# Performance work log

Measured on AMD Instinct MI355X. Metric: run time of the kernel, lower is better.

Reference implementation:

```python
import jax, jax.numpy as jnp
from jax import lax
import numpy as np

Z, Y, X = 41, 256, 256  # sparse_shape = grid_size[::-1]
N_VOX = 60000
C_IN = 4
DN = ('NCDHW', 'OIDHW', 'NCDHW')


def _conv(x, w, stride=(1, 1, 1), pad=1):
    return lax.conv_general_dilated(x, w, stride, [(pad, pad)] * 3, dimension_numbers=DN)


def _tconv(x, w, stride=(2, 2, 2), pad=1, outpad=(0, 0, 0)):
    # torch ConvTranspose3d (weight [Cin,Cout,k,k,k]) == conv with lhs dilation,
    # spatially-flipped, in/out-swapped kernel, padding (k-1-p, k-1-p+output_padding)
    wt = jnp.flip(jnp.swapaxes(w, 0, 1), axis=(2, 3, 4))
    padding = [(2 - pad, 2 - pad + op) for op in outpad]  # k=3
    return lax.conv_general_dilated(x, wt, (1, 1, 1), padding, lhs_dilation=stride, dimension_numbers=DN)


def _bn_relu(y, s, b, m):
    # eval-mode BN folded into per-channel scale/shift, then ReLU, then restrict
    # to the sparse active-site mask (spconv only stores features at active sites)
    return jax.nn.relu(y * s[None, :, None, None, None] + b[None, :, None, None, None]) * m


def _forward(feats, params, coords, batch_size):
    (w1, s1, b1, w2a, s2a, b2a, w2b, s2b, b2b, w3a, s3a, b3a, w3b, s3b, b3b,
     w4a, s4a, b4a, w4b, s4b, b4b, w5a, s5a, b5a, w5b, s5b, b5b) = params
    B = batch_size
    bi, zi, yi, xi = coords[:, 0], coords[:, 1], coords[:, 2], coords[:, 3]
    dense = jnp.zeros((B, C_IN, Z, Y, X), feats.dtype).at[bi, :, zi, yi, xi].set(feats)
    m0 = jnp.zeros((B, 1, Z, Y, X), feats.dtype).at[bi, 0, zi, yi, xi].set(1.0)
    one = jnp.ones((1, 1, 3, 3, 3), feats.dtype)
    # conv1: SparseConv3d k3 s1 p1 -> active set dilates
    m1 = (_conv(m0, one) > 0).astype(feats.dtype)
    x = _bn_relu(_conv(dense, w1), s1, b1, m1)
    # conv2: SparseConv3d s2 + SubMConv3d (mask unchanged for subm)
    m2 = (_conv(m1, one, (2, 2, 2)) > 0).astype(feats.dtype)
    x = _bn_relu(_conv(x, w2a, (2, 2, 2)), s2a, b2a, m2)
    x = _bn_relu(_conv(x, w2b), s2b, b2b, m2)
    # conv3
    m3 = (_conv(m2, one, (2, 2, 2)) > 0).astype(feats.dtype)
    x = _bn_relu(_conv(x, w3a, (2, 2, 2)), s3a, b3a, m3)
    x = _bn_relu(_conv(x, w3b), s3b, b3b, m3)
    # deconv4: SparseConvTranspose3d s2 + subm
    m4 = (_tconv(m3, one) > 0).astype(feats.dtype)
    x = _bn_relu(_tconv(x, w4a), s4a, b4a, m4)
    x = _bn_relu(_conv(x, w4b), s4b, b4b, m4)
    # deconv5: output_padding (0,3,3) restores full Y/X resolution
    m5 = (_tconv(m4, one, outpad=(0, 3, 3)) > 0).astype(feats.dtype)
    x = _bn_relu(_tconv(x, w5a, outpad=(0, 3, 3)), s5a, b5a, m5)
    x = _bn_relu(_conv(x, w5b), s5b, b5b, m5)
    return x  # dense [B, 32, Z, Y, X]; zeros at inactive sites


def setup_inputs() -> dict:
    rng = np.random.default_rng(0)
    flat = rng.choice(Z * Y * X, size=N_VOX, replace=False)
    zi = (flat // (Y * X)).astype(np.int32)
    rem = flat % (Y * X)
    yi = (rem // X).astype(np.int32)
    xi = (rem % X).astype(np.int32)
    coords = np.stack([np.zeros(N_VOX, np.int32), zi, yi, xi], axis=1)

    def w(o, i):
        return jnp.asarray((rng.standard_normal((o, i, 3, 3, 3)) * 0.05).astype(np.float32))

    def scale(c):
        return jnp.asarray(rng.uniform(0.5, 1.5, c).astype(np.float32))

    def shift(c):
        return jnp.asarray((rng.standard_normal(c) * 0.1).astype(np.float32))

    return {
        'occ_voxel_features': jnp.asarray(rng.standard_normal((N_VOX, C_IN)).astype(np.float32)),
        'occ_voxel_coords': jnp.asarray(coords),
        'batch_size': 1,
        'w1': w(16, 4), 's1': scale(16), 'b1': shift(16),
        'w2a': w(32, 16), 's2a': scale(32), 'b2a': shift(32),
        'w2b': w(32, 32), 's2b': scale(32), 'b2b': shift(32),
        'w3a': w(64, 32), 's3a': scale(64), 'b3a': shift(64),
        'w3b': w(64, 64), 's3b': scale(64), 'b3b': shift(64),
        'w4a': w(64, 32), 's4a': scale(32), 'b4a': shift(32),  # transpose weight [Cin,Cout,...]
        'w4b': w(32, 32), 's4b': scale(32), 'b4b': shift(32),
        'w5a': w(32, 32), 's5a': scale(32), 'b5a': shift(32),
        'w5b': w(32, 32), 's5b': scale(32), 'b5b': shift(32),
    }


def reference(occ_voxel_features, occ_voxel_coords, batch_size,
              w1, s1, b1, w2a, s2a, b2a, w2b, s2b, b2b,
              w3a, s3a, b3a, w3b, s3b, b3b,
              w4a, s4a, b4a, w4b, s4b, b4b,
              w5a, s5a, b5a, w5b, s5b, b5b):
    params = (w1, s1, b1, w2a, s2a, b2a, w2b, s2b, b2b, w3a, s3a, b3a, w3b, s3b, b3b,
              w4a, s4a, b4a, w4b, s4b, b4b, w5a, s5a, b5a, w5b, s5b, b5b)
    return _forward(occ_voxel_features, params, occ_voxel_coords, batch_size)
```

## Files before the change

### kernel.cpp

```cpp
#include <hip/hip_runtime.h>
#include <hip/hip_bf16.h>
#include <stdint.h>

namespace {

constexpr int Z0 = 41, Y0 = 256, X0 = 256;
constexpr int Z2 = 21, Y2 = 128, X2 = 128;
constexpr int Z3 = 11, Y3 = 64,  X3 = 64;
constexpr int Z4 = 21, Y4 = 127, X4 = 127;
constexpr int NV0 = Z0 * Y0 * X0;
constexpr int NV2 = Z2 * Y2 * X2;
constexpr int NV3 = Z3 * Y3 * X3;
constexpr int NV4 = Z4 * Y4 * X4;

constexpr int ZP0 = 43, YP0 = 258, XP0 = 258; constexpr int NP0 = ZP0 * YP0 * XP0;
constexpr int ZP2 = 23, YP2 = 130, XP2 = 130; constexpr int NP2 = ZP2 * YP2 * XP2;
constexpr int ZP3 = 13, YP3 = 66,  XP3 = 66;  constexpr int NP3 = ZP3 * YP3 * XP3;
constexpr int ZP4 = 23, YP4 = 129, XP4 = 129; constexpr int NP4 = ZP4 * YP4 * XP4;

using bf16 = __hip_bfloat16;
typedef __attribute__((ext_vector_type(8))) short s16x8;
typedef __attribute__((ext_vector_type(4))) float f32x4;
typedef __attribute__((ext_vector_type(16))) float f32x16;
typedef __attribute__((ext_vector_type(4))) unsigned u32x4;

__device__ inline unsigned f2b(float f) {
    return (unsigned)__builtin_bit_cast(unsigned short, __float2bfloat16(f));
}

__device__ inline int xcd_swz(int bid, int nwg) {
    int q = nwg >> 3, r = nwg & 7;
    int x = bid & 7, j = bid >> 3;
    return (x < r ? x * (q + 1) : r * (q + 1) + (x - r) * q) + j;
}

__device__ inline void glds16(const bf16* g, void* l) {
    __builtin_amdgcn_global_load_lds(
        (const __attribute__((address_space(1))) void*)g,
        (__attribute__((address_space(3))) void*)l, 16, 0, 0);
}

__global__ __launch_bounds__(256) void sentinel_k(float* out) { out[0] = 12345.0f; }

__global__ __launch_bounds__(256) void scatter_k(const float* __restrict__ feats,
                                                 const int* __restrict__ coords,
                                                 bf16* __restrict__ dense,
                                                 uint8_t* __restrict__ m0, int n) {
    int v = blockIdx.x * 256 + threadIdx.x;
    if (v >= n) return;
    int z = coords[v * 4 + 1], y = coords[v * 4 + 2], x = coords[v * 4 + 3];
    m0[(z * Y0 + y) * X0 + x] = 1;
    int pp = ((z + 1) * YP0 + (y + 1)) * XP0 + (x + 1);
    uint2 u;
    u.x = f2b(feats[v * 4 + 0]) | (f2b(feats[v * 4 + 1]) << 16);
    u.y = f2b(feats[v * 4 + 2]) | (f2b(feats[v * 4 + 3]) << 16);
    *(uint2*)(dense + (size_t)pp * 4) = u;
}

template <int C>
__global__ __launch_bounds__(256) void halo_zero_k(bf16* __restrict__ buf,
                                                   int Zi, int Yi, int Xi,
                                                   int Zp, int Yp, int Xp) {
    int i = blockIdx.x * 256 + threadIdx.x;
    int tot = Zp * Yp * Xp;
    if (i >= tot) return;
    int x = i % Xp; int t = i / Xp; int y = t % Yp; int z = t / Yp;
    bool halo = (z < 1) | (z > Zi) | (y < 1) | (y > Yi) | (x < 1) | (x > Xi);
    if (!halo) return;
    uint4 zz = make_uint4(0, 0, 0, 0);
    uint4* p = (uint4*)(buf + (size_t)i * C);
#pragma unroll
    for (int j = 0; j < C / 8; ++j) p[j] = zz;
}

__global__ __launch_bounds__(256) void repack_frag_k(const float* __restrict__ w,
                                                     bf16* __restrict__ wf,
                                                     int CIN, int COUT, int TRANS) {
    int NT = COUT / 16, KT = CIN / 32;
    int i = blockIdx.x * 256 + threadIdx.x;
    int total = 27 * NT * KT * 64;
    if (i >= total) return;
    int lane = i & 63; int t = i >> 6;
    int kt = t % KT; t /= KT; int nt = t % NT; int tap = t / NT;
    int co = nt * 16 + (lane & 15);
    int ci0 = kt * 32 + (lane >> 4) * 8;
    unsigned e[8];
#pragma unroll
    for (int j = 0; j < 8; ++j) {
        int ci = ci0 + j;
        int src = TRANS ? ((ci * COUT + co) * 27 + tap) : ((co * CIN + ci) * 27 + tap);
        e[j] = f2b(w[src]);
    }
    uint4 u;
    u.x = e[0] | (e[1] << 16); u.y = e[2] | (e[3] << 16);
    u.z = e[4] | (e[5] << 16); u.w = e[6] | (e[7] << 16);
    ((uint4*)wf)[i] = u;
}

__global__ __launch_bounds__(256) void repack_frag32_k(const float* __restrict__ w,
                                                       bf16* __restrict__ wf) {
    int i = blockIdx.x * 256 + threadIdx.x;
    if (i >= 27 * 2 * 64) return;
    int lane = i & 63; int t2 = i >> 6;
    int ks = t2 & 1; int tap = t2 >> 1;
    int co = lane & 31; int h = lane >> 5;
    unsigned e[8];
#pragma unroll
    for (int j = 0; j < 8; ++j) {
        int cin = ks * 16 + h * 8 + j;
        e[j] = f2b(w[(co * 32 + cin) * 27 + tap]);
    }
    uint4 u;
    u.x = e[0] | (e[1] << 16); u.y = e[2] | (e[3] << 16);
    u.z = e[4] | (e[5] << 16); u.w = e[6] | (e[7] << 16);
    ((uint4*)wf)[i] = u;
}

__global__ __launch_bounds__(256) void repack_frag_c16_k(const float* __restrict__ w,
                                                         bf16* __restrict__ wf) {
    int i = blockIdx.x * 256 + threadIdx.x;
    int total = 14 * 2 * 64;
    if (i >= total) return;
    int lane = i & 63; int t = i >> 6;
    int nt = t & 1; int p = t >> 1;
    int lg = lane >> 4, lr = lane & 15;
    int co = nt * 16 + lr;
    unsigned e[8];
#pragma unroll
    for (int j = 0; j < 8; ++j) {
        int tap = 2 * p + (lg >> 1);
        int ci = (lg & 1) * 8 + j;
        e[j] = (tap < 27) ? f2b(w[(co * 16 + ci) * 27 + tap]) : 0u;
    }
    uint4 u;
    u.x = e[0] | (e[1] << 16); u.y = e[2] | (e[3] << 16);
    u.z = e[4] | (e[5] << 16); u.w = e[6] | (e[7] << 16);
    ((uint4*)wf)[i] = u;
}

__global__ __launch_bounds__(256) void repack_frag_l1_k(const float* __restrict__ w,
                                                        bf16* __restrict__ wf) {
    int i = blockIdx.x * 256 + threadIdx.x;
    if (i >= 256) return;
    int lane = i & 63, kb = i >> 6;
    int lg = lane >> 4, lr = lane & 15;
    unsigned e[8];
#pragma unroll
    for (int j = 0; j < 8; ++j) {
        int tap = kb * 8 + lg * 2 + (j >> 2);
        int ci = j & 3;
        e[j] = (tap < 27) ? f2b(w[(lr * 4 + ci) * 27 + tap]) : 0u;
    }
    uint4 u;
    u.x = e[0] | (e[1] << 16); u.y = e[2] | (e[3] << 16);
    u.z = e[4] | (e[5] << 16); u.w = e[6] | (e[7] << 16);
    ((uint4*)wf)[i] = u;
}

__global__ __launch_bounds__(256) void dilate_k(const uint8_t* __restrict__ in,
                                                uint8_t* __restrict__ out,
                                                int Zi, int Yi, int Xi,
                                                int Zo, int Yo, int Xo, int stride) {
    int idx = blockIdx.x * 256 + threadIdx.x;
    int total = Zo * Yo * Xo;
    if (idx >= total) return;
    int x = idx % Xo; int t = idx / Xo; int y = t % Yo; int z = t / Yo;
    int YX = Yi * Xi;
    uint8_t r = 0;
    for (int kz = 0; kz < 3; ++kz) {
        int zi = z * stride + kz - 1;
        if ((unsigned)zi >= (unsigned)Zi) continue;
        for (int ky = 0; ky < 3; ++ky) {
            int yi = y * stride + ky - 1;
            if ((unsigned)yi >= (unsigned)Yi) continue;
            for (int kx = 0; kx < 3; ++kx) {
                int xi = x * stride + kx - 1;
                if ((unsigned)xi >= (unsigned)Xi) continue;
                r |= in[zi * YX + yi * Xi + xi];
            }
        }
    }
    out[idx] = r ? 1 : 0;
}

__global__ __launch_bounds__(256) void dilate4_k(const uint8_t* __restrict__ in,
                                                 uint8_t* __restrict__ out,
                                                 int Z, int Y, int X) {
    int ngx = X >> 2;
    int g = blockIdx.x * 256 + threadIdx.x;
    int total = Z * Y * ngx;
    if (g >= total) return;
    int gx = g % ngx; int t = g / ngx; int y = t % Y; int z = t / Y;
    const int YX = Y * X;
    unsigned r = 0;
    for (int kz = 0; kz < 3; ++kz) {
        int zi = z + kz - 1;
        if ((unsigned)zi >= (unsigned)Z) continue;
        for (int ky = 0; ky < 3; ++ky) {
            int yi = y + ky - 1;
            if ((unsigned)yi >= (unsigned)Y) continue;
            const unsigned* rw = (const unsigned*)(in + zi * YX + yi * X);
            unsigned u1 = rw[gx];
            unsigned u0 = gx ? rw[gx - 1] : 0u;
            unsigned u2 = (gx + 1 < ngx) ? rw[gx + 1] : 0u;
            r |= u1 | ((u1 << 8) | (u0 >> 24)) | ((u1 >> 8) | (u2 << 24));
        }
    }
    r |= r >> 4; r |= r >> 2; r |= r >> 1; r &= 0x01010101u;
    ((unsigned*)out)[g] = r;
}

__global__ __launch_bounds__(256) void tdilate_k(const uint8_t* __restrict__ in,
                                                 uint8_t* __restrict__ out,
                                                 int Zi, int Yi, int Xi,
                                                 int Zo, int Yo, int Xo) {
    int idx = blockIdx.x * 256 + threadIdx.x;
    int total = Zo * Yo * Xo;
    if (idx >= total) return;
    int x = idx % Xo; int t = idx / Xo; int y = t % Yo; int z = t / Yo;
    int YX = Yi * Xi;
    uint8_t r = 0;
    for (int kz = 0; kz < 3; ++kz) {
        int tz = z + 1 - kz;
        if (tz & 1) continue;
        int zi = tz >> 1;
        if ((unsigned)zi >= (unsigned)Zi) continue;
        for (int ky = 0; ky < 3; ++ky) {
            int ty = y + 1 - ky;
            if (ty & 1) continue;
            int yi = ty >> 1;
            if ((unsigned)yi >= (unsigned)Yi) continue;
            for (int kx = 0; kx < 3; ++kx) {
                int tx = x + 1 - kx;
                if (tx & 1) continue;
                int xi = tx >> 1;
                if ((unsigned)xi >= (unsigned)Xi) continue;
                r |= in[zi * YX + yi * Xi + xi];
            }
        }
    }
    out[idx] = r ? 1 : 0;
}

__global__ __launch_bounds__(256) void tdilate4_k(const uint8_t* __restrict__ in,
                                                  uint8_t* __restrict__ out,
                                                  int Zi, int Yi, int Xi,
                                                  int Zo, int Yo, int Xo) {
    int ngx = Xo >> 2;
    int g = blockIdx.x * 256 + threadIdx.x;
    int total = Zo * Yo * ngx;
    if (g >= total) return;
    int gx = g % ngx; int t = g / ngx; int y = t % Yo; int z = t / Yo;
    int YX = Yi * Xi;
    int j0 = gx * 2;
    unsigned r0 = 0, r1 = 0, r2 = 0, r3 = 0;
    for (int kz = 0; kz < 3; ++kz) {
        int tz = z + 1 - kz;
        if (tz & 1) continue;
        int zi = tz >> 1;
        if ((unsigned)zi >= (unsigned)Zi) continue;
        for (int ky = 0; ky < 3; ++ky) {
            int ty = y + 1 - ky;
            if (ty & 1) continue;
            int yi = ty >> 1;
            if ((unsigned)yi >= (unsigned)Yi) continue;
            const uint8_t* rp = in + zi * YX + yi * Xi;
            unsigned b0 = (j0 < Xi) ? rp[j0] : 0u;
            unsigned b1 = (j0 + 1 < Xi) ? rp[j0 + 1] : 0u;
            unsigned b2 = (j0 + 2 < Xi) ? rp[j0 + 2] : 0u;
            r0 |= b0; r1 |= b0 | b1; r2 |= b1; r3 |= b1 | b2;
        }
    }
    unsigned rr = (r0 ? 1u : 0u) | (r1 ? 0x100u : 0u) | (r2 ? 0x10000u : 0u) | (r3 ? 0x1000000u : 0u);
    ((unsigned*)out)[g] = rr;
}

__global__ __launch_bounds__(256, 1) void conv_roll_k(
    const bf16* __restrict__ in, const bf16* __restrict__ wfrag,
    const float* __restrict__ scale, const float* __restrict__ shift,
    const uint8_t* __restrict__ mask, float* __restrict__ outf) {
    constexpr int ROWB = 2176;
    constexpr int SLABB = 24576;
    __shared__ uint4 ring4[4 * SLABB / 16];
    char* ring = (char*)ring4;

    const int bid = xcd_swz(blockIdx.x, gridDim.x);
    const int tx = bid & 7;
    const int t2 = bid >> 3;
    const int ty = t2 & 31;
    const int zs = t2 >> 5;
    const int y0 = ty * 8, x0 = tx * 32;
    const int zlo = zs ? 21 : 0;
    const int zcnt = zs ? 20 : 21;

    const int tid = threadIdx.x;
    const int w = tid >> 6, lane = tid & 63;
    const int vx = lane & 31, h = lane >> 5;

#pragma unroll
    for (int k = 0; k < 14; ++k) {
        int base = k * 256 + w * 64;
        if (base < 27 * 2 * 64)
            glds16(wfrag + (size_t)(base + lane) * 8, ring + base * 16);
    }
    asm volatile("s_waitcnt vmcnt(0)" ::: "memory");
    __syncthreads();

    u32x4 breg[27][2];
#pragma unroll
    for (int t = 0; t < 27; ++t) {
        breg[t][0] = *(const u32x4*)(ring + (t * 2 + 0) * 1024 + lane * 16);
        breg[t][1] = *(const u32x4*)(ring + (t * 2 + 1) * 1024 + lane * 16);
    }
    __syncthreads();

    int soff[6];
#pragma unroll
    for (int k = 0; k < 6; ++k) {
        int i = tid + k * 256;
        int ii = i < 1360 ? i : 0;
        int row = ii / 136, c = ii - row * 136;
        int ks = c / 68, r2 = c - ks * 68, hh = r2 / 34, v = r2 - hh * 34;
        soff[k] = ((y0 + row) * XP0 + (x0 + v)) * 32 + (2 * ks + hh) * 8;
    }
    auto stagefn = [&](int p, char* slab) {
        int zp = p < ZP0 ? p : ZP0 - 1;
        const bf16* pb = in + (size_t)zp * ((size_t)YP0 * XP0 * 32);
#pragma unroll
        for (int k = 0; k < 6; ++k)
            glds16(pb + soff[k], slab + (k * 256 + w * 64) * 16);
    };

    int rb[4];
#pragma unroll
    for (int fr = 0; fr < 4; ++fr)
        rb[fr] = (2 * w + fr) * ROWB + h * 544 + vx * 16;

    const float sc = scale[vx], sh = shift[vx];

    stagefn(zlo + 0, ring);
    stagefn(zlo + 1, ring + SLABB);
    stagefn(zlo + 2, ring + 2 * SLABB);
    asm volatile("s_waitcnt vmcnt(0)" ::: "memory");
    __builtin_amdgcn_s_barrier();

    int s0 = 0;
    for (int zi = 0; zi < zcnt; ++zi) {
        const int z = zlo + zi;
        stagefn(z + 3, ring + ((s0 + 3) & 3) * SLABB);

        unsigned mk0[4], mk1[4];
        {
            const uint8_t* mr0 = mask + ((size_t)z * Y0 + (y0 + 2 * w)) * X0 + x0 + 4 * h;
            const uint8_t* mr1 = mr0 + X0;
            mk0[0] = *(const unsigned*)(mr0);      mk0[1] = *(const unsigned*)(mr0 + 8);
            mk0[2] = *(const unsigned*)(mr0 + 16); mk0[3] = *(const unsigned*)(mr0 + 24);
            mk1[0] = *(const unsigned*)(mr1);      mk1[1] = *(const unsigned*)(mr1 + 8);
            mk1[2] = *(const unsigned*)(mr1 + 16); mk1[3] = *(const unsigned*)(mr1 + 24);
        }

        const char* slp0 = ring + s0 * SLABB;
        const char* slp1 = ring + ((s0 + 1) & 3) * SLABB;
        const char* slp2 = ring + ((s0 + 2) & 3) * SLABB;

        f32x16 acc0, acc1;
#pragma unroll
        for (int i = 0; i < 16; ++i) { acc0[i] = 0.f; acc1[i] = 0.f; }

#pragma unroll
        for (int dz = 0; dz < 3; ++dz) {
            const char* slab = dz == 0 ? slp0 : (dz == 1 ? slp1 : slp2);
#pragma unroll
            for (int dx = 0; dx < 3; ++dx) {
#pragma unroll
                for (int ks = 0; ks < 2; ++ks) {
                    const int ko = ks * 1088 + dx * 16;
                    u32x4 a0 = *(const u32x4*)(slab + rb[0] + ko);
                    u32x4 a1 = *(const u32x4*)(slab + rb[1] + ko);
                    u32x4 a2 = *(const u32x4*)(slab + rb[2] + ko);
                    u32x4 a3 = *(const u32x4*)(slab + rb[3] + ko);
                    const int t0 = dz * 9 + 0 * 3 + dx;
                    const int t1 = dz * 9 + 1 * 3 + dx;
                    const int t2_ = dz * 9 + 2 * 3 + dx;
                    acc0 = __builtin_amdgcn_mfma_f32_32x32x16_bf16(
                        __builtin_bit_cast(s16x8, a0), __builtin_bit_cast(s16x8, breg[t0][ks]), acc0, 0, 0, 0);
                    acc1 = __builtin_amdgcn_mfma_f32_32x32x16_bf16(
                        __builtin_bit_cast(s16x8, a1), __builtin_bit_cast(s16x8, breg[t0][ks]), acc1, 0, 0, 0);
                    acc0 = __builtin_amdgcn_mfma_f32_32x32x16_bf16(
                        __builtin_bit_cast(s16x8, a1), __builtin_bit_cast(s16x8, breg[t1][ks]), acc0, 0, 0, 0);
                    acc1 = __builtin_amdgcn_mfma_f32_32x32x16_bf16(
                        __builtin_bit_cast(s16x8, a2), __builtin_bit_cast(s16x8, breg[t1][ks]), acc1, 0, 0, 0);
                    acc0 = __builtin_amdgcn_mfma_f32_32x32x16_bf16(
                        __builtin_bit_cast(s16x8, a2), __builtin_bit_cast(s16x8, breg[t2_][ks]), acc0, 0, 0, 0);
                    acc1 = __builtin_amdgcn_mfma_f32_32x32x16_bf16(
                        __builtin_bit_cast(s16x8, a3), __builtin_bit_cast(s16x8, breg[t2_][ks]), acc1, 0, 0, 0);
                }
            }
        }

        const size_t ob0 = (size_t)vx * NV0 + ((size_t)z * Y0 + (y0 + 2 * w)) * X0 + x0 + 4 * h;
        const size_t ob1 = ob0 + X0;
#pragma unroll
        for (int q = 0; q < 4; ++q) {
            f32x4 o0, o1;
#pragma unroll
            for (int r = 0; r < 4; ++r) {
                float m0 = (float)((mk0[q] >> (8 * r)) & 1);
                float m1 = (float)((mk1[q] >> (8 * r)) & 1);
                o0[r] = fmaxf(fmaf(acc0[q * 4 + r], sc, sh), 0.f) * m0;
                o1[r] = fmaxf(fmaf(acc1[q * 4 + r], sc, sh), 0.f) * m1;
            }
            *(f32x4*)(outf + ob0 + 8 * q) = o0;
            *(f32x4*)(outf + ob1 + 8 * q) = o1;
        }

        asm volatile("s_waitcnt vmcnt(8)" ::: "memory");
        __builtin_amdgcn_s_barrier();
        s0 = (s0 + 1) & 3;
    }
}

__global__ __launch_bounds__(256, 3) void tconv_roll_k(
    const bf16* __restrict__ in, const bf16* __restrict__ wfrag,
    const float* __restrict__ scale, const float* __restrict__ shift,
    const uint8_t* __restrict__ mask, bf16* __restrict__ out,
    int Zo, int Yo, int Xo, int Zi, int Ypi, int Xpi, int Ypo, int Xpo, int nx) {
    constexpr int ROWB = 34 * 64;
    constexpr int SLABB = 3 * ROWB;
    __shared__ uint4 ring4[4 * SLABB / 16];
    char* ring = (char*)ring4;

    const int oct = blockIdx.y;
    const int pz = oct >> 2, py = (oct >> 1) & 1, px = oct & 1;
    const int Zq = (Zo - pz + 1) >> 1;

    const int bid = xcd_swz(blockIdx.x, gridDim.x);
    const int tx = bid % nx, ty = bid / nx;
    const int yq0 = ty * 2, xq0 = tx * 32;

    const int tid = threadIdx.x;
    const int w = tid >> 6, lane = tid & 63;
    const int lg = lane >> 4, lr = lane & 15;
    const int yr = w >> 1, xh = w & 1;

    const int kz0 = pz ? 0 : 1, dzo0 = pz ? 1 : 0;
    const int ky0 = py ? 0 : 1, dyo0 = py ? 1 : 0;
    const int kx0 = px ? 0 : 1, dxo0 = px ? 1 : 0;

    auto stagefn = [&](int p, int slot) {
        if (w < 3) {
            int zs = p < Zi ? p : Zi - 1;
            char* slab = ring + slot * SLABB + w * ROWB;
            const bf16* pb = in + ((size_t)(zs + 1) * Ypi + (yq0 + 1 + w)) * (size_t)Xpi * 32
                                + (size_t)(xq0 + 1) * 32;
            int u0 = lane;      glds16(pb + (u0 ^ ((u0 >> 3) & 7)) * 8, slab);
            int u1 = 64 + lane; glds16(pb + (u1 ^ ((u1 >> 3) & 7)) * 8, slab + 1024);
            if (lane < 8) { int u2 = 128 + lane; glds16(pb + u2 * 8, slab + 2048); }
        }
    };

    const uint4* gw = (const uint4*)wfrag;
    uint4 breg[2][2][2][2];
#pragma unroll
    for (int iz = 0; iz < 2; ++iz) {
        int kz = iz ? 2 : kz0;
#pragma unroll
        for (int iy = 0; iy < 2; ++iy) {
            int ky = iy ? 2 : ky0;
#pragma unroll
            for (int ix = 0; ix < 2; ++ix) {
                int kx = ix ? 2 : kx0;
                int tap = kz * 9 + ky * 3 + kx;
                breg[iz][iy][ix][0] = gw[(tap * 2 + 0) * 64 + lane];
                breg[iz][iy][ix][1] = gw[(tap * 2 + 1) * 64 + lane];
            }
        }
    }

    int b0 = (xh * 16 + lr + dxo0) * 64 + lg * 16;
    int b1 = (xh * 16 + lr) * 64 + lg * 16;
    const int aswA = b0 ^ (((b0 >> 7) & 7) << 4);
    const int aswB = b1 ^ (((b1 >> 7) & 7) << 4);
    const int rowA = (yr + dyo0) * ROWB;
    const int rowB = yr * ROWB;

    const float sc0 = scale[lr], sh0 = shift[lr];
    const float sc1 = scale[16 + lr], sh1 = shift[16 + lr];

    const int yout = 2 * (yq0 + yr) + py;
    const int xb = 2 * (xq0 + xh * 16 + lg * 4) + px;

    stagefn(0, 0); stagefn(1, 1); stagefn(2, 2);
    uint2 mv;
    mv = *(const uint2*)(mask + ((size_t)pz * Yo + yout) * Xo + (xb - px));
    asm volatile("s_waitcnt vmcnt(0)" ::: "memory");
    __builtin_amdgcn_s_barrier();

    int rs0 = 0, wslot = 3;
    for (int zq = 0; zq < Zq; ++zq) {
        uint2 nv;
        {
            int zqn = (zq + 1 < Zq) ? zq + 1 : Zq - 1;
            nv = *(const uint2*)(mask + ((size_t)(2 * zqn + pz) * Yo + yout) * Xo + (xb - px));
        }
        stagefn(zq + 3, wslot);

        int rs1 = rs0 + 1 < 4 ? rs0 + 1 : 0;
        const char* sl_0 = ring + rs0 * SLABB;
        const char* sl_1 = ring + rs1 * SLABB;
        const char* slz0 = pz ? sl_1 : sl_0;
        const char* slz1 = sl_0;

        f32x4 acc0 = (f32x4){0, 0, 0, 0}, acc1 = (f32x4){0, 0, 0, 0};
#pragma unroll
        for (int iz = 0; iz < 2; ++iz) {
            if (iz > pz) continue;
            const char* slab = iz ? slz1 : slz0;
#pragma unroll
            for (int iy = 0; iy < 2; ++iy) {
                if (iy > py) continue;
                const char* rowp = slab + (iy ? rowB : rowA);
#pragma unroll
                for (int ix = 0; ix < 2; ++ix) {
                    if (ix > px) continue;
                    uint4 a = *(const uint4*)(rowp + (ix ? aswB : aswA));
                    acc0 = __builtin_amdgcn_mfma_f32_16x16x32_bf16(
                        __builtin_bit_cast(s16x8, a),
                        __builtin_bit_cast(s16x8, breg[iz][iy][ix][0]), acc0, 0, 0, 0);
                    acc1 = __builtin_amdgcn_mfma_f32_16x16x32_bf16(
                        __builtin_bit_cast(s16x8, a),
                        __builtin_bit_cast(s16x8, breg[iz][iy][ix][1]), acc1, 0, 0, 0);
                }
            }
        }

        const int zout = 2 * zq + pz;
        const size_t opdbase = ((size_t)(zout + 1) * Ypo + (yout + 1)) * Xpo;
#pragma unroll
        for (int r = 0; r < 4; ++r) {
            unsigned word = (r < 2) ? mv.x : mv.y;
            float m = (float)((word >> (px * 8 + (r & 1) * 16)) & 1);
            float v0 = fmaxf(fmaf(acc0[r], sc0, sh0), 0.f) * m;
            float v1 = fmaxf(fmaf(acc1[r], sc1, sh1), 0.f) * m;
            size_t opd = opdbase + (size_t)(xb + 2 * r + 1);
            out[opd * 32 + lr]      = __float2bfloat16(v0);
            out[opd * 32 + 16 + lr] = __float2bfloat16(v1);
        }

        asm volatile("s_waitcnt vmcnt(20)" ::: "memory");
        __builtin_amdgcn_s_barrier();
        rs0 = rs1;
        wslot = wslot + 1 < 4 ? wslot + 1 : 0;
        mv = nv;
    }
}

template <bool FINAL>
__global__ __launch_bounds__(512, 4) void conv_lds_k(
    const bf16* __restrict__ in, const bf16* __restrict__ wfrag,
    const float* __restrict__ scale, const float* __restrict__ shift,
    const uint8_t* __restrict__ mask, bf16* __restrict__ out, float* __restrict__ outf,
    int Zo, int Yo, int Xo, int Ypi, int Xpi, int Ypo, int Xpo, int nx, int ny) {
    constexpr int ROWB = 34 * 64;
    __shared__ uint4 tile4[36 * ROWB / 16];
    char* tile = (char*)tile4;

    const int No = Zo * Yo * Xo;
    const int bid = xcd_swz(blockIdx.x, gridDim.x);
    int tx = bid % nx; int tt = bid / nx; int ty = tt % ny; int tz = tt / ny;
    const int z0 = tz * 4, y0 = ty * 4, x0 = tx * 32;

    const int tid = threadIdx.x;
    const int w = tid >> 6, lane = tid & 63, lg = lane >> 4, lr = lane & 15;

    int anywork;
    {
        int row = tid >> 5, xl = tid & 31;
        int zz = z0 + (row >> 2), yy = y0 + (row & 3), xx = x0 + xl;
        int ok = (zz < Zo) && (yy < Yo) && (xx < Xo) && mask[((size_t)zz * Yo + yy) * Xo + xx];
        anywork = __syncthreads_or(ok);
    }

    f32x4 acc[4][2];
#pragma unroll
    for (int s = 0; s < 4; ++s) { acc[s][0] = (f32x4){0,0,0,0}; acc[s][1] = (f32x4){0,0,0,0}; }

    if (anywork) {
        const int lsw = (lane ^ ((lane >> 3) & 7)) * 8;
        for (int rr = w; rr < 36; rr += 8) {
            int dz = rr / 6, dy = rr % 6;
            const bf16* g = in + ((size_t)(z0 + dz) * Ypi + (y0 + dy)) * Xpi * 32 + (size_t)x0 * 32;
            char* l = tile + rr * ROWB;
            glds16(g + lsw, l);
            glds16(g + 512 + lsw, l + 1024);
            if (lane < 8) glds16(g + 1024 + lane * 8, l + 2048);
        }
        asm volatile("s_waitcnt vmcnt(0)" ::: "memory");
        __syncthreads();

        int rbB[4], bsw[4][3];
#pragma unroll
        for (int s = 0; s < 4; ++s) {
            int lrow = 2 * w + (s >> 1);
            rbB[s] = ((lrow >> 2) * 6 + (lrow & 3)) * ROWB;
            int xpart = (s & 1) * 16 + lr;
#pragma unroll
            for (int dx = 0; dx < 3; ++dx) {
                int b = (xpart + dx) * 64 + lg * 16;
                bsw[s][dx] = b ^ (((b >> 7) & 7) << 4);
            }
        }

        const uint4* gw = (const uint4*)wfrag;
#pragma unroll 1
        for (int dz = 0; dz < 3; ++dz) {
#pragma unroll
            for (int dy = 0; dy < 3; ++dy) {
                const int rowoff = (dz * 6 + dy) * ROWB;
#pragma unroll
                for (int dx = 0; dx < 3; ++dx) {
                    const int tap = dz * 9 + dy * 3 + dx;
                    uint4 b0 = gw[(tap * 2 + 0) * 64 + lane];
                    uint4 b1 = gw[(tap * 2 + 1) * 64 + lane];
                    uint4 ua[4];
#pragma unroll
                    for (int s = 0; s < 4; ++s)
                        ua[s] = *(const uint4*)(tile + rbB[s] + rowoff + bsw[s][dx]);
#pragma unroll
                    for (int s = 0; s < 4; ++s) {
                        acc[s][0] = __builtin_amdgcn_mfma_f32_16x16x32_bf16(
                            __builtin_bit_cast(s16x8, ua[s]),
                            __builtin_bit_cast(s16x8, b0), acc[s][0], 0, 0, 0);
                        acc[s][1] = __builtin_amdgcn_mfma_f32_16x16x32_bf16(
                            __builtin_bit_cast(s16x8, ua[s]),
                            __builtin_bit_cast(s16x8, b1), acc[s][1], 0, 0, 0);
                    }
                }
            }
        }
    }

#pragma unroll
    for (int s = 0; s < 4; ++s) {
        int lrow = 2 * w + (s >> 1);
        int zz = z0 + (lrow >> 2), yy = y0 + (lrow & 3);
        int xv = x0 + (s & 1) * 16 + lg * 4;
        bool rowok = (zz < Zo) && (yy < Yo);
        if (!rowok) continue;
        size_t idx0 = ((size_t)zz * Yo + yy) * Xo + xv;
        float mm[4];
#pragma unroll
        for (int r = 0; r < 4; ++r)
            mm[r] = (xv + r < Xo && mask[idx0 + r]) ? 1.f : 0.f;
        if constexpr (FINAL) {
#pragma unroll
            for (int nt = 0; nt < 2; ++nt) {
                int co = nt * 16 + lr;
                float sc = scale[co], sh = shift[co];
                f32x4 o;
#pragma unroll
                for (int r = 0; r < 4; ++r)
                    o[r] = fmaxf(fmaf(acc[s][nt][r], sc, sh), 0.f) * mm[r];
                if (xv + 3 < Xo) {
                    *(f32x4*)(outf + (size_t)co * No + idx0) = o;
                } else {
#pragma unroll
                    for (int r = 0; r < 4; ++r)
                        if (xv + r < Xo) outf[(size_t)co * No + idx0 + r] = o[r];
                }
            }
        } else {
            int opd = ((zz + 1) * Ypo + (yy + 1)) * Xpo + (xv + 1);
#pragma unroll
            for (int nt = 0; nt < 2; ++nt) {
                int co = nt * 16 + lr;
                float sc = scale[co], sh = shift[co];
#pragma unroll
                for (int r = 0; r < 4; ++r) {
                    if (xv + r >= Xo) continue;
                    float yv = fmaxf(fmaf(acc[s][nt][r], sc, sh), 0.f) * mm[r];
                    out[(size_t)(opd + r) * 32 + co] = __float2bfloat16(yv);
                }
            }
        }
    }
}

template <int CIN, int COUT, int STRIDE, int BLK, bool FINAL>
__global__ __launch_bounds__(BLK, ((CIN <= 32 && COUT <= 32) ? 4 : 2)) void conv_mfma_k(
    const bf16* __restrict__ in, const bf16* __restrict__ wfrag,
    const float* __restrict__ scale, const float* __restrict__ shift,
    const uint8_t* __restrict__ mask, bf16* __restrict__ out, float* __restrict__ outf,
    int Zo, int Yo, int Xo, int Ypi, int Xpi, int Ypo, int Xpo) {
    constexpr int NT = COUT / 16;
    constexpr int KT = CIN / 32;
    const int No = Zo * Yo * Xo;
    const int bid = xcd_swz(blockIdx.x, gridDim.x);
    const int tid = threadIdx.x;
    const int wv = tid >> 6, lane = tid & 63;
    const int lg = lane >> 4, lr = lane & 15;
    const int v0 = bid * BLK + wv * 64;
    if (v0 >= No) return;

    int vm = v0 + lane;
    bool mw = (vm < No) && (mask[vm] != 0);
    const bool anywork = (__ballot(mw) != 0ull);

    f32x4 acc[4][NT];
#pragma unroll
    for (int s = 0; s < 4; ++s)
#pragma unroll
        for (int nt = 0; nt < NT; ++nt) acc[s][nt] = (f32x4){0.f, 0.f, 0.f, 0.f};

    const uint4* gw = (const uint4*)wfrag;

    if (anywork) {
        int pA[4];
#pragma unroll
        for (int s = 0; s < 4; ++s) {
            int vr = v0 + s * 16 + lr;
            if (vr >= No) vr = 0;
            int zz = vr / (Yo * Xo); int rr = vr - zz * (Yo * Xo);
            int yy = rr / Xo; int xx = rr - yy * Xo;
            pA[s] = (((zz * STRIDE + 1) * Ypi + (yy * STRIDE + 1)) * Xpi + (xx * STRIDE + 1)) * CIN + lg * 8;
        }
#pragma unroll
        for (int tap = 0; tap < 27; ++tap) {
            const int kz = tap / 9, r9 = tap - kz * 9, ky = r9 / 3, kx = r9 - ky * 3;
            const int toff = (((kz - 1) * Ypi + (ky - 1)) * Xpi + (kx - 1)) * CIN;
            uint4 ub[NT][KT];
#pragma unroll
            for (int nt = 0; nt < NT; ++nt)
#pragma unroll
                for (int kt = 0; kt < KT; ++kt)
                    ub[nt][kt] = gw[((tap * NT + nt) * KT + kt) * 64 + lane];
            uint4 ua[4][KT];
#pragma unroll
            for (int s = 0; s < 4; ++s)
#pragma unroll
                for (int kt = 0; kt < KT; ++kt)
                    ua[s][kt] = *(const uint4*)(in + pA[s] + toff + kt * 32);
#pragma unroll
            for (int s = 0; s < 4; ++s)
#pragma unroll
                for (int kt = 0; kt < KT; ++kt)
#pragma unroll
                    for (int nt = 0; nt < NT; ++nt)
                        acc[s][nt] = __builtin_amdgcn_mfma_f32_16x16x32_bf16(
                            __builtin_bit_cast(s16x8, ua[s][kt]),
                            __builtin_bit_cast(s16x8, ub[nt][kt]), acc[s][nt], 0, 0, 0);
        }
    }

#pragma unroll
    for (int s = 0; s < 4; ++s) {
        const int vb = v0 + s * 16 + lg * 4;
        int opd[4]; float mm[4]; bool ok[4];
#pragma unroll
        for (int r = 0; r < 4; ++r) {
            int v = vb + r;
            ok[r] = v < No;
            int vc = ok[r] ? v : 0;
            mm[r] = (ok[r] && mask[vc]) ? 1.f : 0.f;
            int zz = vc / (Yo * Xo); int rr = vc - zz * (Yo * Xo);
            int yy = rr / Xo; int xx = rr - yy * Xo;
            opd[r] = FINAL ? vc : ((zz + 1) * Ypo + (yy + 1)) * Xpo + (xx + 1);
        }
#pragma unroll
        for (int nt = 0; nt < NT; ++nt) {
            int co = nt * 16 + lr;
            float sc = scale[co], sh = shift[co];
#pragma unroll
            for (int r = 0; r < 4; ++r) {
                if (!ok[r]) continue;
                float yv = fmaxf(fmaf(acc[s][nt][r], sc, sh), 0.f) * mm[r];
                if constexpr (FINAL) outf[(size_t)co * No + opd[r]] = yv;
                else out[(size_t)opd[r] * COUT + co] = __float2bfloat16(yv);
            }
        }
    }
}

__global__ __launch_bounds__(256, 4) void conv_s2c16_k(
    const bf16* __restrict__ in, const bf16* __restrict__ wfrag,
    const float* __restrict__ scale, const float* __restrict__ shift,
    const uint8_t* __restrict__ mask, bf16* __restrict__ out,
    int Zo, int Yo, int Xo, int Ypi, int Xpi, int Ypo, int Xpo) {
    const int No = Zo * Yo * Xo;
    const int bid = xcd_swz(blockIdx.x, gridDim.x);
    const int tid = threadIdx.x;
    const int wv = tid >> 6, lane = tid & 63;
    const int lg = lane >> 4, lr = lane & 15;
    const int v0 = bid * 256 + wv * 64;
    if (v0 >= No) return;

    int vm = v0 + lane;
    bool mw = (vm < No) && (mask[vm] != 0);
    const bool anywork = (__ballot(mw) != 0ull);

    f32x4 acc[4][2];
#pragma unroll
    for (int s = 0; s < 4; ++s) { acc[s][0] = (f32x4){0,0,0,0}; acc[s][1] = (f32x4){0,0,0,0}; }

    if (anywork) {
        const uint4* gw = (const uint4*)wfrag;
        const int choff = (lg & 1) * 8;
        const int tb = lg >> 1;
        int toffl[14];
#pragma unroll
        for (int p = 0; p < 14; ++p) {
            int tp = 2 * p + tb;
            if (tp >= 27) tp = 0;
            int kz = tp / 9, r9 = tp - kz * 9, ky = r9 / 3, kx = r9 - ky * 3;
            toffl[p] = ((kz * Ypi + ky) * Xpi + kx) * 16;
        }
        int pA[4];
#pragma unroll
        for (int s = 0; s < 4; ++s) {
            int vr = v0 + s * 16 + lr;
            if (vr >= No) vr = 0;
            int zz = vr / (Yo * Xo); int rr = vr - zz * (Yo * Xo);
            int yy = rr / Xo; int xx = rr - yy * Xo;
            pA[s] = (((zz * 2) * Ypi + (yy * 2)) * Xpi + (xx * 2)) * 16 + choff;
        }
#pragma unroll
        for (int p = 0; p < 14; ++p) {
            uint4 b0 = gw[(p * 2 + 0) * 64 + lane];
            uint4 b1 = gw[(p * 2 + 1) * 64 + lane];
            uint4 ua[4];
#pragma unroll
            for (int s = 0; s < 4; ++s)
                ua[s] = *(const uint4*)(in + pA[s] + toffl[p]);
#pragma unroll
            for (int s = 0; s < 4; ++s) {
                acc[s][0] = __builtin_amdgcn_mfma_f32_16x16x32_bf16(
                    __builtin_bit_cast(s16x8, ua[s]),
                    __builtin_bit_cast(s16x8, b0), acc[s][0], 0, 0, 0);
                acc[s][1] = __builtin_amdgcn_mfma_f32_16x16x32_bf16(
                    __builtin_bit_cast(s16x8, ua[s]),
                    __builtin_bit_cast(s16x8, b1), acc[s][1], 0, 0, 0);
            }
        }
    }

#pragma unroll
    for (int s = 0; s < 4; ++s) {
        const int vb = v0 + s * 16 + lg * 4;
        int opd[4]; float mm[4]; bool ok[4];
#pragma unroll
        for (int r = 0; r < 4; ++r) {
            int v = vb + r;
            ok[r] = v < No;
            int vc = ok[r] ? v : 0;
            mm[r] = (ok[r] && mask[vc]) ? 1.f : 0.f;
            int zz = vc / (Yo * Xo); int rr = vc - zz * (Yo * Xo);
            int yy = rr / Xo; int xx = rr - yy * Xo;
            opd[r] = ((zz + 1) * Ypo + (yy + 1)) * Xpo + (xx + 1);
        }
#pragma unroll
        for (int nt = 0; nt < 2; ++nt) {
            int co = nt * 16 + lr;
            float sc = scale[co], sh = shift[co];
#pragma unroll
            for (int r = 0; r < 4; ++r) {
                if (!ok[r]) continue;
                float yv = fmaxf(fmaf(acc[s][nt][r], sc, sh), 0.f) * mm[r];
                out[(size_t)opd[r] * 32 + co] = __float2bfloat16(yv);
            }
        }
    }
}

template <int CIN, int COUT>
__global__ __launch_bounds__(256, 4) void tconv_mfma_k(
    const bf16* __restrict__ in, const bf16* __restrict__ wfrag,
    const float* __restrict__ scale, const float* __restrict__ shift,
    const uint8_t* __restrict__ mask, bf16* __restrict__ out,
    int Zo, int Yo, int Xo, int Ypi, int Xpi, int Ypo, int Xpo) {
    constexpr int NT = COUT / 16;
    constexpr int KT = CIN / 32;
    const int oct = blockIdx.y;
    const int pz = oct >> 2, py = (oct >> 1) & 1, px = oct & 1;
    const int Zq = (Zo - pz + 1) >> 1, Yq = (Yo - py + 1) >> 1, Xq = (Xo - px + 1) >> 1;
    const int Nq = Zq * Yq * Xq;
    const int YXq = Yq * Xq;
    const int bid = xcd_swz(blockIdx.x, gridDim.x);
    const int tid = threadIdx.x;
    const int wv = tid >> 6, lane = tid & 63;
    const int lg = lane >> 4, lr = lane & 15;
    const int v0 = bid * 256 + wv * 64;
    if (v0 >= Nq) return;

    bool mw = false;
    {
        int q = v0 + lane;
        if (q < Nq) {
            int zq = q / YXq; int rr = q - zq * YXq; int yq = rr / Xq; int xq = rr - yq * Xq;
            int zz = 2 * zq + pz, yy = 2 * yq + py, xx = 2 * xq + px;
            mw = mask[(zz * Yo + yy) * Xo + xx] != 0;
        }
    }
    const bool anywork = (__ballot(mw) != 0ull);

    f32x4 acc[4][NT];
#pragma unroll
    for (int s = 0; s < 4; ++s)
#pragma unroll
        for (int nt = 0; nt < NT; ++nt) acc[s][nt] = (f32x4){0.f, 0.f, 0.f, 0.f};

    const uint4* gw = (const uint4*)wfrag;

    if (anywork) {
        int pA[4];
#pragma unroll
        for (int s = 0; s < 4; ++s) {
            int q = v0 + s * 16 + lr;
            if (q >= Nq) q = 0;
            int zq = q / YXq; int rr = q - zq * YXq; int yq = rr / Xq; int xq = rr - yq * Xq;
            pA[s] = (((zq + 1) * Ypi + (yq + 1)) * Xpi + (xq + 1)) * CIN + lg * 8;
        }
        const int nkz = 1 + pz, nky = 1 + py, nkx = 1 + px;
        for (int iz = 0; iz < nkz; ++iz) {
            const int kz = pz ? (iz ? 2 : 0) : 1;
            const int dz = (pz && !iz) ? 1 : 0;
            for (int iy = 0; iy < nky; ++iy) {
                const int ky = py ? (iy ? 2 : 0) : 1;
                const int dy = (py && !iy) ? 1 : 0;
                for (int ix = 0; ix < nkx; ++ix) {
                    const int kx = px ? (ix ? 2 : 0) : 1;
                    const int dx = (px && !ix) ? 1 : 0;
                    const int tap = kz * 9 + ky * 3 + kx;
                    const int toff = ((dz * Ypi + dy) * Xpi + dx) * CIN;
                    uint4 ub[NT][KT];
#pragma unroll
                    for (int nt = 0; nt < NT; ++nt)
#pragma unroll
                        for (int kt = 0; kt < KT; ++kt)
                            ub[nt][kt] = gw[((tap * NT + nt) * KT + kt) * 64 + lane];
                    uint4 ua[4][KT];
#pragma unroll
                    for (int s = 0; s < 4; ++s)
#pragma unroll
                        for (int kt = 0; kt < KT; ++kt)
                            ua[s][kt] = *(const uint4*)(in + pA[s] + toff + kt * 32);
#pragma unroll
                    for (int s = 0; s < 4; ++s)
#pragma unroll
                        for (int kt = 0; kt < KT; ++kt)
#pragma unroll
                            for (int nt = 0; nt < NT; ++nt)
                                acc[s][nt] = __builtin_amdgcn_mfma_f32_16x16x32_bf16(
                                    __builtin_bit_cast(s16x8, ua[s][kt]),
                                    __builtin_bit_cast(s16x8, ub[nt][kt]), acc[s][nt], 0, 0, 0);
                }
            }
        }
    }

#pragma unroll
    for (int s = 0; s < 4; ++s) {
        const int vb = v0 + s * 16 + lg * 4;
        int opd[4]; float mm[4]; bool ok[4];
#pragma unroll
        for (int r = 0; r < 4; ++r) {
            int q = vb + r;
            ok[r] = q < Nq;
            int qc = ok[r] ? q : 0;
            int zq = qc / YXq; int rr = qc - zq * YXq; int yq = rr / Xq; int xq = rr - yq * Xq;
            int zz = 2 * zq + pz, yy = 2 * yq + py, xx = 2 * xq + px;
            mm[r] = (ok[r] && mask[(zz * Yo + yy) * Xo + xx]) ? 1.f : 0.f;
            opd[r] = ((zz + 1) * Ypo + (yy + 1)) * Xpo + (xx + 1);
        }
#pragma unroll
        for (int nt = 0; nt < NT; ++nt) {
            int co = nt * 16 + lr;
            float sc = scale[co], sh = shift[co];
#pragma unroll
            for (int r = 0; r < 4; ++r) {
                if (!ok[r]) continue;
                float yv = fmaxf(fmaf(acc[s][nt][r], sc, sh), 0.f) * mm[r];
                out[(size_t)opd[r] * COUT + co] = __float2bfloat16(yv);
            }
        }
    }
}

__global__ __launch_bounds__(256, 4) void conv_l1_mfma_k(
    const bf16* __restrict__ in, const bf16* __restrict__ wfrag,
    const float* __restrict__ scale, const float* __restrict__ shift,
    const uint8_t* __restrict__ mask, bf16* __restrict__ out,
    int Zo, int Yo, int Xo, int Ypi, int Xpi, int Ypo, int Xpo) {
    const int No = Zo * Yo * Xo;
    const int bid = xcd_swz(blockIdx.x, gridDim.x);
    const int tid = threadIdx.x;
    const int wv = tid >> 6, lane = tid & 63;
    const int lg = lane >> 4, lr = lane & 15;
    const int v0 = bid * 256 + wv * 64;
    if (v0 >= No) return;

    int vm = v0 + lane;
    bool mw = (vm < No) && (mask[vm] != 0);
    const bool anywork = (__ballot(mw) != 0ull);

    f32x4 acc[4];
#pragma unroll
    for (int s = 0; s < 4; ++s) acc[s] = (f32x4){0.f, 0.f, 0.f, 0.f};

    if (anywork) {
        const uint4* gw = (const uint4*)wfrag;
        uint4 bu[4];
#pragma unroll
        for (int kb = 0; kb < 4; ++kb) bu[kb] = gw[kb * 64 + lane];

        int vtf[4][2];
#pragma unroll
        for (int kb = 0; kb < 4; ++kb)
#pragma unroll
            for (int u = 0; u < 2; ++u) {
                int tp = kb * 8 + lg * 2 + u;
                int kz = tp / 9, r9 = tp - kz * 9, ky = r9 / 3, kx = r9 - ky * 3;
                vtf[kb][u] = (tp < 27) ? (((kz - 1) * Ypi + (ky - 1)) * Xpi + (kx - 1)) : 0;
            }

        int pV[4];
#pragma unroll
        for (int s = 0; s < 4; ++s) {
            int vr = v0 + s * 16 + lr;
            if (vr >= No) vr = 0;
            int zz = vr / (Yo * Xo); int rr = vr - zz * (Yo * Xo);
            int yy = rr / Xo; int xx = rr - yy * Xo;
            pV[s] = ((zz + 1) * Ypi + (yy + 1)) * Xpi + (xx + 1);
        }

#pragma unroll
        for (int kb = 0; kb < 4; ++kb) {
#pragma unroll
            for (int s = 0; s < 4; ++s) {
                uint2 a0 = *(const uint2*)(in + (size_t)(pV[s] + vtf[kb][0]) * 4);
                uint2 a1 = *(const uint2*)(in + (size_t)(pV[s] + vtf[kb][1]) * 4);
                int4 ai; ai.x = a0.x; ai.y = a0.y; ai.z = a1.x; ai.w = a1.y;
                acc[s] = __builtin_amdgcn_mfma_f32_16x16x32_bf16(
                    __builtin_bit_cast(s16x8, ai),
                    __builtin_bit_cast(s16x8, bu[kb]), acc[s], 0, 0, 0);
            }
        }
    }

#pragma unroll
    for (int s = 0; s < 4; ++s) {
        const int vb = v0 + s * 16 + lg * 4;
        int co = lr;
        float sc = scale[co], sh = shift[co];
#pragma unroll
        for (int r = 0; r < 4; ++r) {
            int v = vb + r;
            if (v >= No) continue;
            float mm = mask[v] ? 1.f : 0.f;
            int zz = v / (Yo * Xo); int rr = v - zz * (Yo * Xo);
            int yy = rr / Xo; int xx = rr - yy * Xo;
            int opd = ((zz + 1) * Ypo + (yy + 1)) * Xpo + (xx + 1);
            float yv = fmaxf(fmaf(acc[s][r], sc, sh), 0.f) * mm;
            out[(size_t)opd * 16 + co] = __float2bfloat16(yv);
        }
    }
}

inline int nblk(int n) { return (n + 255) / 256; }
inline int cdiv(int a, int b) { return (a + b - 1) / b; }

}

extern "C" void kernel_launch(void* const* d_in, const int* in_sizes, int n_in,
                              void* d_out, int out_size, void* d_ws, size_t ws_size,
                              hipStream_t stream) {
    const float* feats = (const float*)d_in[0];
    const int* coords = (const int*)d_in[1];
    const int NVOX = in_sizes[0] / 4;

    const float *w1 = (const float*)d_in[3], *s1 = (const float*)d_in[4], *b1 = (const float*)d_in[5];
    const float *w2a = (const float*)d_in[6], *s2a = (const float*)d_in[7], *b2a = (const float*)d_in[8];
    const float *w2b = (const float*)d_in[9], *s2b = (const float*)d_in[10], *b2b = (const float*)d_in[11];
    const float *w3a = (const float*)d_in[12], *s3a = (const float*)d_in[13], *b3a = (const float*)d_in[14];
    const float *w3b = (const float*)d_in[15], *s3b = (const float*)d_in[16], *b3b = (const float*)d_in[17];
    const float *w4a = (const float*)d_in[18], *s4a = (const float*)d_in[19], *b4a = (const float*)d_in[20];
    const float *w4b = (const float*)d_in[21], *s4b = (const float*)d_in[22], *b4b = (const float*)d_in[23];
    const float *w5a = (const float*)d_in[24], *s5a = (const float*)d_in[25], *b5a = (const float*)d_in[26];
    const float *w5b = (const float*)d_in[27], *s5b = (const float*)d_in[28], *b5b = (const float*)d_in[29];

    char* ws = (char*)d_ws;
    size_t off = 0;
    auto alloc = [&](size_t bytes) -> void* {
        void* p = ws + off;
        off = (off + bytes + 255) & ~(size_t)255;
        return p;
    };

    uint8_t* m0 = (uint8_t*)alloc(NV0);
    uint8_t* m1 = (uint8_t*)alloc(NV0);
    uint8_t* m2 = (uint8_t*)alloc(NV2);
    uint8_t* m3 = (uint8_t*)alloc(NV3);
    uint8_t* m4 = (uint8_t*)alloc(NV4);
    uint8_t* m5 = (uint8_t*)alloc(NV0);

    bf16* slot0 = (bf16*)alloc((size_t)NP0 * 32 * 2);
    bf16* slot1 = (bf16*)alloc((size_t)NP0 * 16 * 2);

    bf16* dense0 = slot0;
    bf16* x1     = slot1;
    bf16* x2a    = slot0;
    bf16* x2b    = slot1;
    bf16* x3a    = slot0;
    bf16* x3b    = slot1;
    bf16* x4a    = slot0;
    bf16* x4b    = slot1;
    bf16* x5a    = slot0;

    bf16* wfL1 = (bf16*)alloc(4 * 64 * 8 * 2);
    bf16* wf2a = (bf16*)alloc((size_t)14 * 2 * 64 * 16);
    bf16* wf2b = (bf16*)alloc((size_t)27 * 2 * 1 * 64 * 16);
    bf16* wf3a = (bf16*)alloc((size_t)27 * 4 * 1 * 64 * 16);
    bf16* wf3b = (bf16*)alloc((size_t)27 * 4 * 2 * 64 * 16);
    bf16* wf4a = (bf16*)alloc((size_t)27 * 2 * 2 * 64 * 16);
    bf16* wf4b = (bf16*)alloc((size_t)27 * 2 * 1 * 64 * 16);
    bf16* wf5a = (bf16*)alloc((size_t)27 * 2 * 1 * 64 * 16);
    bf16* wf5b32 = (bf16*)alloc((size_t)27 * 2 * 64 * 16);
    alloc(20u << 20);

    if (off > ws_size) {
        sentinel_k<<<1, 256, 0, stream>>>((float*)d_out);
        return;
    }

    hipMemsetAsync(dense0, 0, (size_t)NP0 * 4 * 2, stream);
    hipMemsetAsync(m0, 0, NV0, stream);
    repack_frag_l1_k<<<1, 256, 0, stream>>>(w1, wfL1);
    repack_frag_c16_k<<<nblk(14 * 2 * 64), 256, 0, stream>>>(w2a, wf2a);
    repack_frag_k<<<nblk(27 * 2 * 64), 256, 0, stream>>>(w2b, wf2b, 32, 32, 0);
    repack_frag_k<<<nblk(27 * 4 * 64), 256, 0, stream>>>(w3a, wf3a, 32, 64, 0);
    repack_frag_k<<<nblk(27 * 8 * 64), 256, 0, stream>>>(w3b, wf3b, 64, 64, 0);
    repack_frag_k<<<nblk(27 * 4 * 64), 256, 0, stream>>>(w4a, wf4a, 64, 32, 1);
    repack_frag_k<<<nblk(27 * 2 * 64), 256, 0, stream>>>(w4b, wf4b, 32, 32, 0);
    repack_frag_k<<<nblk(27 * 2 * 64), 256, 0, stream>>>(w5a, wf5a, 32, 32, 1);
    repack_frag32_k<<<nblk(27 * 2 * 64), 256, 0, stream>>>(w5b, wf5b32);

    scatter_k<<<nblk(NVOX), 256, 0, stream>>>(feats, coords, dense0, m0, NVOX);

    dilate4_k<<<nblk(NV0 / 4), 256, 0, stream>>>(m0, m1, Z0, Y0, X0);
    halo_zero_k<16><<<nblk(NP0), 256, 0, stream>>>(x1, Z0, Y0, X0, ZP0, YP0, XP0);
    conv_l1_mfma_k<<<nblk(NV0), 256, 0, stream>>>(
        dense0, wfL1, s1, b1, m1, x1, Z0, Y0, X0, YP0, XP0, YP0, XP0);

    dilate_k<<<nblk(NV2), 256, 0, stream>>>(m1, m2, Z0, Y0, X0, Z2, Y2, X2, 2);
    halo_zero_k<32><<<nblk(NP2), 256, 0, stream>>>(x2a, Z2, Y2, X2, ZP2, YP2, XP2);
    conv_s2c16_k<<<nblk(NV2), 256, 0, stream>>>(
        x1, wf2a, s2a, b2a, m2, x2a, Z2, Y2, X2, YP0, XP0, YP2, XP2);
    halo_zero_k<32><<<nblk(NP2), 256, 0, stream>>>(x2b, Z2, Y2, X2, ZP2, YP2, XP2);
    {
        int nx = cdiv(X2, 32), ny = cdiv(Y2, 4), nz = cdiv(Z2, 4);
        conv_lds_k<false><<<nx * ny * nz, 512, 0, stream>>>(
            x2a, wf2b, s2b, b2b, m2, x2b, nullptr, Z2, Y2, X2, YP2, XP2, YP2, XP2, nx, ny);
    }

    dilate_k<<<nblk(NV3), 256, 0, stream>>>(m2, m3, Z2, Y2, X2, Z3, Y3, X3, 2);
    halo_zero_k<64><<<nblk(NP3), 256, 0, stream>>>(x3a, Z3, Y3, X3, ZP3, YP3, XP3);
    conv_mfma_k<32, 64, 2, 64, false><<<cdiv(NV3, 64), 64, 0, stream>>>(
        x2b, wf3a, s3a, b3a, m3, x3a, nullptr, Z3, Y3, X3, YP2, XP2, YP3, XP3);
    halo_zero_k<64><<<nblk(NP3), 256, 0, stream>>>(x3b, Z3, Y3, X3, ZP3, YP3, XP3);
    conv_mfma_k<64, 64, 1, 64, false><<<cdiv(NV3, 64), 64, 0, stream>>>(
        x3a, wf3b, s3b, b3b, m3, x3b, nullptr, Z3, Y3, X3, YP3, XP3, YP3, XP3);

    tdilate_k<<<nblk(NV4), 256, 0, stream>>>(m3, m4, Z3, Y3, X3, Z4, Y4, X4);
    halo_zero_k<32><<<nblk(NP4), 256, 0, stream>>>(x4a, Z4, Y4, X4, ZP4, YP4, XP4);
    {
        int maxNq = ((Z4 + 1) >> 1) * ((Y4 + 1) >> 1) * ((X4 + 1) >> 1);
        dim3 g(nblk(maxNq), 8);
        tconv_mfma_k<64, 32><<<g, 256, 0, stream>>>(
            x3b, wf4a, s4a, b4a, m4, x4a, Z4, Y4, X4, YP3, XP3, YP4, XP4);
    }
    halo_zero_k<32><<<nblk(NP2), 256, 0, stream>>>(x4b, Z4, Y4, X4, ZP2, YP2, XP2);
    {
        int nx = cdiv(X4, 32), ny = cdiv(Y4, 4), nz = cdiv(Z4, 4);
        conv_lds_k<false><<<nx * ny * nz, 512, 0, stream>>>(
            x4a, wf4b, s4b, b4b, m4, x4b, nullptr, Z4, Y4, X4, YP4, XP4, YP2, XP2, nx, ny);
    }

    tdilate4_k<<<nblk(NV0 / 4), 256, 0, stream>>>(m4, m5, Z4, Y4, X4, Z0, Y0, X0);
    halo_zero_k<32><<<nblk(NP0), 256, 0, stream>>>(x5a, Z0, Y0, X0, ZP0, YP0, XP0);
    {
        dim3 g((Y0 / 2 / 2) * (X0 / 2 / 32), 8);
        tconv_roll_k<<<g, 256, 0, stream>>>(
            x4b, wf5a, s5a, b5a, m5, x5a, Z0, Y0, X0, Z4, YP2, XP2, YP0, XP0, X0 / 2 / 32);
    }
    {
        conv_roll_k<<<512, 256, 0, stream>>>(
            x5a, wf5b32, s5b, b5b, m5, (float*)d_out);
    }
}
```

Baseline: 797.9 us.

## Pair output channels in tconv stores and drop z-split in final conv

The weight repack for the last transposed conv now interleaves output channels so that each lane holds channels 2c and 2c+1. The epilogue can then write both bf16 results as one packed 32-bit store instead of two 16-bit stores, and the vmcnt wait threshold is lowered to match the smaller number of outstanding stores. Separately, the final conv_roll kernel no longer splits the z range across two blocks; it launches half as many blocks, each walking all 41 z slices. This removes duplicated halo staging and prologue work but halves the parallelism of that kernel.

```diff
diff --git a/kernel.cpp b/kernel.cpp
--- a/kernel.cpp
+++ b/kernel.cpp
@@ -75,14 +75,15 @@
 
 __global__ __launch_bounds__(256) void repack_frag_k(const float* __restrict__ w,
                                                      bf16* __restrict__ wf,
-                                                     int CIN, int COUT, int TRANS) {
+                                                     int CIN, int COUT, int TRANS, int PAIR) {
     int NT = COUT / 16, KT = CIN / 32;
     int i = blockIdx.x * 256 + threadIdx.x;
     int total = 27 * NT * KT * 64;
     if (i >= total) return;
     int lane = i & 63; int t = i >> 6;
     int kt = t % KT; t /= KT; int nt = t % NT; int tap = t / NT;
-    int co = nt * 16 + (lane & 15);
+    int c = lane & 15;
+    int co = PAIR ? (2 * c + nt) : (nt * 16 + c);
     int ci0 = kt * 32 + (lane >> 4) * 8;
     unsigned e[8];
 #pragma unroll
@@ -285,13 +286,8 @@
     char* ring = (char*)ring4;
 
     const int bid = xcd_swz(blockIdx.x, gridDim.x);
-    const int tx = bid & 7;
-    const int t2 = bid >> 3;
-    const int ty = t2 & 31;
-    const int zs = t2 >> 5;
+    const int tx = bid & 7, ty = bid >> 3;
     const int y0 = ty * 8, x0 = tx * 32;
-    const int zlo = zs ? 21 : 0;
-    const int zcnt = zs ? 20 : 21;
 
     const int tid = threadIdx.x;
     const int w = tid >> 6, lane = tid & 63;
@@ -338,15 +334,14 @@
 
     const float sc = scale[vx], sh = shift[vx];
 
-    stagefn(zlo + 0, ring);
-    stagefn(zlo + 1, ring + SLABB);
-    stagefn(zlo + 2, ring + 2 * SLABB);
+    stagefn(0, ring);
+    stagefn(1, ring + SLABB);
+    stagefn(2, ring + 2 * SLABB);
     asm volatile("s_waitcnt vmcnt(0)" ::: "memory");
     __builtin_amdgcn_s_barrier();
 
     int s0 = 0;
-    for (int zi = 0; zi < zcnt; ++zi) {
-        const int z = zlo + zi;
+    for (int z = 0; z < Z0; ++z) {
         stagefn(z + 3, ring + ((s0 + 3) & 3) * SLABB);
 
         unsigned mk0[4], mk1[4];
@@ -484,8 +479,8 @@
     const int rowA = (yr + dyo0) * ROWB;
     const int rowB = yr * ROWB;
 
-    const float sc0 = scale[lr], sh0 = shift[lr];
-    const float sc1 = scale[16 + lr], sh1 = shift[16 + lr];
+    const float sc0 = scale[2 * lr], sh0 = shift[2 * lr];
+    const float sc1 = scale[2 * lr + 1], sh1 = shift[2 * lr + 1];
 
     const int yout = 2 * (yq0 + yr) + py;
     const int xb = 2 * (xq0 + xh * 16 + lg * 4) + px;
@@ -543,11 +538,11 @@
             float v0 = fmaxf(fmaf(acc0[r], sc0, sh0), 0.f) * m;
             float v1 = fmaxf(fmaf(acc1[r], sc1, sh1), 0.f) * m;
             size_t opd = opdbase + (size_t)(xb + 2 * r + 1);
-            out[opd * 32 + lr]      = __float2bfloat16(v0);
-            out[opd * 32 + 16 + lr] = __float2bfloat16(v1);
-        }
-
-        asm volatile("s_waitcnt vmcnt(20)" ::: "memory");
+            unsigned pk = f2b(v0) | (f2b(v1) << 16);
+            *(unsigned*)(out + opd * 32 + 2 * lr) = pk;
+        }
+
+        asm volatile("s_waitcnt vmcnt(12)" ::: "memory");
         __builtin_amdgcn_s_barrier();
         rs0 = rs1;
         wslot = wslot + 1 < 4 ? wslot + 1 : 0;
@@ -1135,12 +1130,12 @@
     hipMemsetAsync(m0, 0, NV0, stream);
     repack_frag_l1_k<<<1, 256, 0, stream>>>(w1, wfL1);
     repack_frag_c16_k<<<nblk(14 * 2 * 64), 256, 0, stream>>>(w2a, wf2a);
-    repack_frag_k<<<nblk(27 * 2 * 64), 256, 0, stream>>>(w2b, wf2b, 32, 32, 0);
-    repack_frag_k<<<nblk(27 * 4 * 64), 256, 0, stream>>>(w3a, wf3a, 32, 64, 0);
-    repack_frag_k<<<nblk(27 * 8 * 64), 256, 0, stream>>>(w3b, wf3b, 64, 64, 0);
-    repack_frag_k<<<nblk(27 * 4 * 64), 256, 0, stream>>>(w4a, wf4a, 64, 32, 1);
-    repack_frag_k<<<nblk(27 * 2 * 64), 256, 0, stream>>>(w4b, wf4b, 32, 32, 0);
-    repack_frag_k<<<nblk(27 * 2 * 64), 256, 0, stream>>>(w5a, wf5a, 32, 32, 1);
+    repack_frag_k<<<nblk(27 * 2 * 64), 256, 0, stream>>>(w2b, wf2b, 32, 32, 0, 0);
+    repack_frag_k<<<nblk(27 * 4 * 64), 256, 0, stream>>>(w3a, wf3a, 32, 64, 0, 0);
+    repack_frag_k<<<nblk(27 * 8 * 64), 256, 0, stream>>>(w3b, wf3b, 64, 64, 0, 0);
+    repack_frag_k<<<nblk(27 * 4 * 64), 256, 0, stream>>>(w4a, wf4a, 64, 32, 1, 0);
+    repack_frag_k<<<nblk(27 * 2 * 64), 256, 0, stream>>>(w4b, wf4b, 32, 32, 0, 0);
+    repack_frag_k<<<nblk(27 * 2 * 64), 256, 0, stream>>>(w5a, wf5a, 32, 32, 1, 1);
     repack_frag32_k<<<nblk(27 * 2 * 64), 256, 0, stream>>>(w5b, wf5b32);
 
     scatter_k<<<nblk(NVOX), 256, 0, stream>>>(feats, coords, dense0, m0, NVOX);
@@ -1192,7 +1187,7 @@
             x4b, wf5a, s5a, b5a, m5, x5a, Z0, Y0, X0, Z4, YP2, XP2, YP0, XP0, X0 / 2 / 32);
     }
     {
-        conv_roll_k<<<512, 256, 0, stream>>>(
+        conv_roll_k<<<256, 256, 0, stream>>>(
             x5a, wf5b32, s5b, b5b, m5, (float*)d_out);
     }
 }
```

Result: no change. 789.7 us (-1.0%).
